# Performance work log

Measured on AMD Instinct MI355X. Metric: run time of the kernel, lower is better.

Reference implementation:

```python
import jax, jax.numpy as jnp
import numpy as np

N = 50000
E_RAND = 800000
F_IN = 128
HID = 128
HEADS = 8
LAYERS = 2
DH = HID // HEADS  # 16


def setup_inputs() -> dict:
    key = jax.random.key(0)
    ks = jax.random.split(key, 8)
    x = jax.random.normal(ks[0], (N, F_IN), dtype=jnp.float32)
    # random edges + self loops so every row of the segment-softmax is nonempty
    rnd = jax.random.randint(ks[1], (2, E_RAND), 0, N, dtype=jnp.int32)
    loops = jnp.tile(jnp.arange(N, dtype=jnp.int32), (2, 1))
    edge_idx = jnp.concatenate([rnd, loops], axis=1)  # [2, 850000]
    edge_vals = jnp.ones((edge_idx.shape[1],), dtype=jnp.float32)
    # glorot-style params
    enc_W = jax.random.normal(ks[2], (F_IN, HID), dtype=jnp.float32) * np.sqrt(2.0 / (F_IN + HID))
    enc_b = jnp.zeros((HID,), dtype=jnp.float32)
    W_stack = jax.random.normal(ks[3], (LAYERS, HEADS, HID, DH), dtype=jnp.float32) * np.sqrt(2.0 / (HID + DH))
    a_stack = jax.random.normal(ks[4], (LAYERS, HEADS, 2 * DH), dtype=jnp.float32) * np.sqrt(2.0 / (1 + 2 * DH))
    return {"x": x, "edge_idx": edge_idx, "edge_vals": edge_vals,
            "enc_W": enc_W, "enc_b": enc_b, "W_stack": W_stack, "a_stack": a_stack}


def _gat_layer(xin, row, col, edge_vals, W, a):
    # xin: [N, HID]; W: [H, HID, DH]; a: [H, 2*DH]
    n = xin.shape[0]
    h = jnp.einsum('nd,hdf->hnf', xin, W)            # [H, N, DH]
    a_src, a_dst = a[:, :DH], a[:, DH:]
    alpha_src = jnp.einsum('hnf,hf->hn', h, a_src)   # a . h[row] part
    alpha_dst = jnp.einsum('hnf,hf->hn', h, a_dst)   # a . h[col] part
    logits = edge_vals[None, :] * (alpha_src[:, row] + alpha_dst[:, col])  # [H, E]
    e = jnp.exp(jax.nn.leaky_relu(logits, 0.2))      # unnormalized attention
    rowsum = jax.ops.segment_sum(e.T, row, num_segments=n)               # [N, H]
    msg = e[:, :, None] * h[:, col, :]               # [H, E, DH]
    agg = jax.vmap(lambda m: jax.ops.segment_sum(m, row, num_segments=n))(msg)  # [H, N, DH]
    out = agg / rowsum.T[:, :, None]
    return jnp.transpose(out, (1, 0, 2)).reshape(n, -1)  # concat heads -> [N, HID]


def reference(x, edge_idx, edge_vals, enc_W, enc_b, W_stack, a_stack):
    row, col = edge_idx[0], edge_idx[1]
    xc = x @ enc_W + enc_b  # encoder
    L = W_stack.shape[0]
    for ell in range(L):
        out = _gat_layer(xc, row, col, edge_vals, W_stack[ell], a_stack[ell])
        if ell != L - 1:
            out = jax.nn.elu(out)  # feat_drop is identity in eval mode
        xc = out + xc if ell > 0 else out  # use_residual=True
    # single snapshot: stack over T=1 then permute(1,0,2) -> [N, 1, HID]
    return xc[:, None, :]
```

## Files before the change

kernel.cpp:

```cpp
#include <hip/hip_runtime.h>
#include <hip/hip_bf16.h>


typedef __attribute__((ext_vector_type(8))) short short8;
typedef __attribute__((ext_vector_type(4))) float floatx4;
typedef __attribute__((ext_vector_type(2))) float floatx2;

__device__ __forceinline__ unsigned f2u(float f) { return __float_as_uint(f); }
__device__ __forceinline__ float u2f(unsigned u) { return __uint_as_float(u); }
__device__ __forceinline__ unsigned short f2bf_rne(float x) {
    unsigned u = f2u(x);
    unsigned r = (u + 0x7FFF + ((u >> 16) & 1)) >> 16;
    return (unsigned short)r;
}
__device__ __forceinline__ float bf2f(unsigned short b) { return u2f(((unsigned)b) << 16); }


__global__ void hist_kernel(const int* __restrict__ row, int* __restrict__ deg,
                            int* __restrict__ rank, int E) {
    int e = blockIdx.x * 256 + threadIdx.x;
    if (e < E) rank[e] = atomicAdd(&deg[row[e]], 1);
}

__global__ void blocksum_kernel(const int* __restrict__ deg, int* __restrict__ bsum, int n) {
    __shared__ int sd[512];
    int t = threadIdx.x;
    int idx = blockIdx.x * 512 + t;
    sd[t] = (idx < n) ? deg[idx] : 0;
    __syncthreads();
    for (int off = 256; off; off >>= 1) {
        if (t < off) sd[t] += sd[t + off];
        __syncthreads();
    }
    if (t == 0) bsum[blockIdx.x] = sd[0];
}

__global__ void scanbsum_kernel(const int* __restrict__ bsum, int* __restrict__ boff,
                                int nb, int* __restrict__ rowptr, int n) {
    __shared__ int sd[128];
    int t = threadIdx.x;
    int v = (t < nb) ? bsum[t] : 0;
    sd[t] = v;
    __syncthreads();
    for (int off = 1; off < 128; off <<= 1) {
        int add = (t >= off) ? sd[t - off] : 0;
        __syncthreads();
        sd[t] += add;
        __syncthreads();
    }
    if (t < nb) boff[t] = sd[t] - v;
    if (t == nb - 1) rowptr[n] = sd[t];
}

__global__ void scanfinal_kernel(const int* __restrict__ deg, const int* __restrict__ boff,
                                 int* __restrict__ rowptr, int n) {
    __shared__ int sd[512];
    int t = threadIdx.x;
    int idx = blockIdx.x * 512 + t;
    int v = (idx < n) ? deg[idx] : 0;
    sd[t] = v;
    __syncthreads();
    for (int off = 1; off < 512; off <<= 1) {
        int add = (t >= off) ? sd[t - off] : 0;
        __syncthreads();
        sd[t] += add;
        __syncthreads();
    }
    if (idx < n) rowptr[idx] = sd[t] - v + boff[blockIdx.x];
}

__global__ void scatterperm_kernel(const int* __restrict__ row, const int* __restrict__ rank,
                                   const int* __restrict__ rowptr, int* __restrict__ perm,
                                   int E) {
    int e = blockIdx.x * 256 + threadIdx.x;
    if (e < E) perm[rowptr[row[e]] + rank[e]] = e;
}

__global__ void gathercv_kernel(const int* __restrict__ perm, const int* __restrict__ colv,
                                const float* __restrict__ ev, int2* __restrict__ csr_cv,
                                int E) {
    int s = blockIdx.x * 256 + threadIdx.x;
    if (s < E) {
        int e = perm[s];
        csr_cv[s] = make_int2(colv[e], __float_as_int(ev[e]));
    }
}


__global__ void pack_kernel(const float* __restrict__ encW, const float* __restrict__ Wstack,
                            short8* __restrict__ Wh, short8* __restrict__ Wl) {
    int idx = blockIdx.x * 256 + threadIdx.x;
    if (idx >= 3 * 2048) return;
    int mat = idx >> 11;
    int r = idx & 2047;
    int lane = r & 63;
    int tile = r >> 6;
    int ct = tile >> 2, kt = tile & 3;
    int ncol = ct * 16 + (lane & 15);
    int k0 = kt * 32 + ((lane >> 4) * 8);
    short8 hv, lv;
#pragma unroll
    for (int j = 0; j < 8; ++j) {
        int k = k0 + j;
        float w = (mat == 0)
            ? encW[k * 128 + ncol]
            : Wstack[(mat - 1) * 16384 + (ncol >> 4) * 2048 + k * 16 + (ncol & 15)];
        unsigned u = f2u(w);
        hv[j] = (short)(u >> 16);
        float hf = u2f(u & 0xFFFF0000u);
        float l = w - hf;
        lv[j] = (short)(f2u(l) >> 16);
    }
    Wh[idx] = hv;
    Wl[idx] = lv;
}


__global__ __launch_bounds__(256) void
gemm_mfma(const float* __restrict__ A, const short8* __restrict__ Bh,
          const short8* __restrict__ Bl, const float* __restrict__ bias,
          const float* __restrict__ avec, float* __restrict__ Cf,
          unsigned short* __restrict__ Cbf,
          float* __restrict__ asrc, float* __restrict__ adst, int n, int flags) {
    int wave = threadIdx.x >> 6;
    int lane = threadIdx.x & 63;
    int q = lane >> 4;
    int col = lane & 15;
    int n0w = blockIdx.x * 64 + wave * 16;

    int arow = min(n0w + col, n - 1);
    const float* Arow = A + (size_t)arow * 128;
    int kb = q * 8;
    short8 Ah[4], Al[4];
#pragma unroll
    for (int kt = 0; kt < 4; ++kt) {
        float4 f0 = *(const float4*)(Arow + kt * 32 + kb);
        float4 f1 = *(const float4*)(Arow + kt * 32 + kb + 4);
        float fv[8] = {f0.x, f0.y, f0.z, f0.w, f1.x, f1.y, f1.z, f1.w};
#pragma unroll
        for (int j = 0; j < 8; ++j) {
            unsigned u = f2u(fv[j]);
            Ah[kt][j] = (short)(u >> 16);
            float hf = u2f(u & 0xFFFF0000u);
            float l = fv[j] - hf;
            Al[kt][j] = (short)(f2u(l) >> 16);
        }
    }

    int nbase = n0w + q * 4;
#pragma unroll
    for (int ct = 0; ct < 8; ++ct) {
        short8 bh[4], bl[4];
#pragma unroll
        for (int kt = 0; kt < 4; ++kt) {
            bh[kt] = Bh[(ct * 4 + kt) * 64 + lane];
            bl[kt] = Bl[(ct * 4 + kt) * 64 + lane];
        }
        float bv = (flags & 1) ? bias[ct * 16 + col] : 0.f;
        floatx4 acc = {bv, bv, bv, bv};
#pragma unroll
        for (int kt = 0; kt < 4; ++kt) {
            acc = __builtin_amdgcn_mfma_f32_16x16x32_bf16(Ah[kt], bh[kt], acc, 0, 0, 0);
            acc = __builtin_amdgcn_mfma_f32_16x16x32_bf16(Al[kt], bh[kt], acc, 0, 0, 0);
            acc = __builtin_amdgcn_mfma_f32_16x16x32_bf16(Ah[kt], bl[kt], acc, 0, 0, 0);
        }
#pragma unroll
        for (int reg = 0; reg < 4; ++reg) {
            int node = nbase + reg;
            if (node < n) {
                if (flags & 4) Cbf[(size_t)node * 128 + ct * 16 + col] = f2bf_rne(acc[reg]);
                else           Cf[(size_t)node * 128 + ct * 16 + col] = acc[reg];
            }
        }
        if (flags & 2) {
            float a_s = avec[ct * 32 + col];
            float a_d = avec[ct * 32 + 16 + col];
#pragma unroll
            for (int reg = 0; reg < 4; ++reg) {
                float ps = acc[reg] * a_s;
                float pd = acc[reg] * a_d;
#pragma unroll
                for (int off = 8; off; off >>= 1) {
                    ps += __shfl_down(ps, off, 16);
                    pd += __shfl_down(pd, off, 16);
                }
                int node = nbase + reg;
                if (col == 0 && node < n) {
                    asrc[node * 8 + ct] = ps;
                    adst[node * 8 + ct] = pd;
                }
            }
        }
    }
}


__global__ __launch_bounds__(256) void
aggregate_kernel(const int* __restrict__ rowptr, const int2* __restrict__ cv,
                 const unsigned short* __restrict__ hbf,
                 const float* __restrict__ asrc, const float* __restrict__ adst,
                 const float* __restrict__ resid, float* __restrict__ out,
                 int mode, int n) {
    int wid = (blockIdx.x * 256 + threadIdx.x) >> 6;
    if (wid >= n) return;
    int lane = threadIdx.x & 63;
    int grp = lane >> 4;
    int l4 = lane & 15;
    int h = l4 >> 1;

    int s = rowptr[wid];
    int e = rowptr[wid + 1];
    float as_w = asrc[wid * 8 + h];

    floatx2 acc0 = {0.f, 0.f}, acc1 = {0.f, 0.f};
    floatx2 acc2 = {0.f, 0.f}, acc3 = {0.f, 0.f};
    float ws = 0.f;

#pragma unroll 4
    for (int j = s + grp; j < e; j += 4) {
        int2 cvj = cv[j];
        int c = cvj.x;
        float v = __int_as_float(cvj.y);
        float lg = v * (as_w + adst[c * 8 + h]);
        float lr = fmaxf(lg, 0.2f * lg);
        float w = __expf(lr);
        uint4 hv = *(const uint4*)(hbf + (size_t)c * 128 + l4 * 8);
        floatx2 w2 = {w, w};
        floatx2 p0 = {u2f(hv.x << 16), u2f(hv.x & 0xFFFF0000u)};
        floatx2 p1 = {u2f(hv.y << 16), u2f(hv.y & 0xFFFF0000u)};
        floatx2 p2 = {u2f(hv.z << 16), u2f(hv.z & 0xFFFF0000u)};
        floatx2 p3 = {u2f(hv.w << 16), u2f(hv.w & 0xFFFF0000u)};
        acc0 += w2 * p0;
        acc1 += w2 * p1;
        acc2 += w2 * p2;
        acc3 += w2 * p3;
        ws += w;
    }

    float a0 = acc0.x, a1 = acc0.y, a2 = acc1.x, a3 = acc1.y;
    float a4 = acc2.x, a5 = acc2.y, a6 = acc3.x, a7 = acc3.y;

#define RED4(x) x += __shfl_xor(x, 16); x += __shfl_xor(x, 32);
    RED4(a0) RED4(a1) RED4(a2) RED4(a3)
    RED4(a4) RED4(a5) RED4(a6) RED4(a7)
    RED4(ws)
#undef RED4

    if (grp == 0) {
        float inv = 1.0f / ws;
        float o[8] = {a0 * inv, a1 * inv, a2 * inv, a3 * inv,
                      a4 * inv, a5 * inv, a6 * inv, a7 * inv};
        size_t base = (size_t)wid * 128 + l4 * 8;
        if (mode == 0) {
#pragma unroll
            for (int k = 0; k < 8; ++k) o[k] = o[k] > 0.f ? o[k] : expm1f(o[k]);
        } else {
            float4 r0 = *(const float4*)(resid + base);
            float4 r1 = *(const float4*)(resid + base + 4);
            o[0] += r0.x; o[1] += r0.y; o[2] += r0.z; o[3] += r0.w;
            o[4] += r1.x; o[5] += r1.y; o[6] += r1.z; o[7] += r1.w;
        }
        float4 w0 = {o[0], o[1], o[2], o[3]};
        float4 w1 = {o[4], o[5], o[6], o[7]};
        *(float4*)(out + base) = w0;
        *(float4*)(out + base + 4) = w1;
    }
}


extern "C" void kernel_launch(void* const* d_in, const int* in_sizes, int n_in,
                              void* d_out, int out_size, void* d_ws, size_t ws_size,
                              hipStream_t stream) {
    const int N = in_sizes[0] / 128;
    const int E = in_sizes[2];

    const float* x      = (const float*)d_in[0];
    const int*   eidx   = (const int*)d_in[1];
    const float* ev     = (const float*)d_in[2];
    const float* encW   = (const float*)d_in[3];
    const float* encb   = (const float*)d_in[4];
    const float* Wstack = (const float*)d_in[5];
    const float* astack = (const float*)d_in[6];
    float* out = (float*)d_out;

    const int* row = eidx;
    const int* colv = eidx + E;

    char* p = (char*)d_ws;
    float* xc   = (float*)p; p += (size_t)N * 128 * 4;
    float* xcB  = (float*)p; p += (size_t)N * 128 * 4;
    unsigned short* hbf = (unsigned short*)p; p += (size_t)N * 128 * 2;
    float* asrc = (float*)p; p += (size_t)N * 8 * 4;
    float* adst = (float*)p; p += (size_t)N * 8 * 4;
    short8* Wh  = (short8*)p; p += 3 * 2048 * 16;
    short8* Wl  = (short8*)p; p += 3 * 2048 * 16;
    int2* csr_cv = (int2*)p; p += (size_t)E * 8;
    int* rowptr = (int*)p;   p += (size_t)(N + 1) * 4;
    int* deg    = (int*)p;   p += (size_t)N * 4;
    int* bsum   = (int*)p;   p += 128 * 4;
    int* boff   = (int*)p;

    int* rank = (int*)xc;
    int* perm = rank + E;

    const int NB = (N + 511) / 512;
    const int GB = (N + 63) / 64;
    const int AGG = (N + 3) / 4;
    const int EB = (E + 255) / 256;

    hipMemsetAsync(deg, 0, (size_t)N * 4, stream);
    hist_kernel<<<EB, 256, 0, stream>>>(row, deg, rank, E);
    blocksum_kernel<<<NB, 512, 0, stream>>>(deg, bsum, N);
    scanbsum_kernel<<<1, 128, 0, stream>>>(bsum, boff, NB, rowptr, N);
    scanfinal_kernel<<<NB, 512, 0, stream>>>(deg, boff, rowptr, N);
    scatterperm_kernel<<<EB, 256, 0, stream>>>(row, rank, rowptr, perm, E);
    gathercv_kernel<<<EB, 256, 0, stream>>>(perm, colv, ev, csr_cv, E);

    pack_kernel<<<24, 256, 0, stream>>>(encW, Wstack, Wh, Wl);

    gemm_mfma<<<GB, 256, 0, stream>>>(x, Wh, Wl, encb, nullptr, xc, nullptr,
                                      nullptr, nullptr, N, 1);

    gemm_mfma<<<GB, 256, 0, stream>>>(xc, Wh + 2048, Wl + 2048, nullptr, astack,
                                      nullptr, hbf, asrc, adst, N, 2 | 4);
    aggregate_kernel<<<AGG, 256, 0, stream>>>(rowptr, csr_cv, hbf, asrc, adst,
                                              nullptr, xcB, 0, N);

    gemm_mfma<<<GB, 256, 0, stream>>>(xcB, Wh + 4096, Wl + 4096, nullptr, astack + 256,
                                      nullptr, hbf, asrc, adst, N, 2 | 4);
    aggregate_kernel<<<AGG, 256, 0, stream>>>(rowptr, csr_cv, hbf, asrc, adst,
                                              xcB, out, 1, N);
}
```

Before: 312.2 us.

## Fuse weight packing into histogram, use atomic-offset scan, prefetch edges in aggregate

Merges the weight-packing kernel into the degree histogram launch as extra blocks. Replaces the three-kernel scan with a single kernel in which each block claims its base offset from a global cursor with an atomic. The resulting row ordering is not sorted by node but is still a valid CSR-like layout, since rows are addressed through rowstart plus degree. The aggregate loop now software-pipelines the edge (col, val) loads four at a time with a prefetch of the next batch, to hide gather latency. The goal is fewer launches and better memory-level parallelism, at the cost of irregular segment placement and more registers.

```diff
diff --git a/kernel.cpp b/kernel.cpp
--- a/kernel.cpp
+++ b/kernel.cpp
@@ -16,45 +16,47 @@
 __device__ __forceinline__ float bf2f(unsigned short b) { return u2f(((unsigned)b) << 16); }
 
 
-__global__ void hist_kernel(const int* __restrict__ row, int* __restrict__ deg,
-                            int* __restrict__ rank, int E) {
-    int e = blockIdx.x * 256 + threadIdx.x;
-    if (e < E) rank[e] = atomicAdd(&deg[row[e]], 1);
-}
-
-__global__ void blocksum_kernel(const int* __restrict__ deg, int* __restrict__ bsum, int n) {
+__global__ void histpack_kernel(const int* __restrict__ row, int* __restrict__ deg,
+                                int* __restrict__ rank, int E, int EB,
+                                const float* __restrict__ encW,
+                                const float* __restrict__ Wstack,
+                                short8* __restrict__ Wh, short8* __restrict__ Wl) {
+    int b = blockIdx.x;
+    if (b < EB) {
+        int e = b * 256 + threadIdx.x;
+        if (e < E) rank[e] = atomicAdd(&deg[row[e]], 1);
+        return;
+    }
+    int idx = (b - EB) * 256 + threadIdx.x;
+    if (idx >= 3 * 2048) return;
+    int mat = idx >> 11;
+    int r = idx & 2047;
+    int lane = r & 63;
+    int tile = r >> 6;
+    int ct = tile >> 2, kt = tile & 3;
+    int ncol = ct * 16 + (lane & 15);
+    int k0 = kt * 32 + ((lane >> 4) * 8);
+    short8 hv, lv;
+#pragma unroll
+    for (int j = 0; j < 8; ++j) {
+        int k = k0 + j;
+        float w = (mat == 0)
+            ? encW[k * 128 + ncol]
+            : Wstack[(mat - 1) * 16384 + (ncol >> 4) * 2048 + k * 16 + (ncol & 15)];
+        unsigned u = f2u(w);
+        hv[j] = (short)(u >> 16);
+        float hf = u2f(u & 0xFFFF0000u);
+        float l = w - hf;
+        lv[j] = (short)(f2u(l) >> 16);
+    }
+    Wh[idx] = hv;
+    Wl[idx] = lv;
+}
+
+__global__ void scan_atomic_kernel(const int* __restrict__ deg, int* __restrict__ rowstart,
+                                   int* __restrict__ gcursor, int n) {
     __shared__ int sd[512];
-    int t = threadIdx.x;
-    int idx = blockIdx.x * 512 + t;
-    sd[t] = (idx < n) ? deg[idx] : 0;
-    __syncthreads();
-    for (int off = 256; off; off >>= 1) {
-        if (t < off) sd[t] += sd[t + off];
-        __syncthreads();
-    }
-    if (t == 0) bsum[blockIdx.x] = sd[0];
-}
-
-__global__ void scanbsum_kernel(const int* __restrict__ bsum, int* __restrict__ boff,
-                                int nb, int* __restrict__ rowptr, int n) {
-    __shared__ int sd[128];
-    int t = threadIdx.x;
-    int v = (t < nb) ? bsum[t] : 0;
-    sd[t] = v;
-    __syncthreads();
-    for (int off = 1; off < 128; off <<= 1) {
-        int add = (t >= off) ? sd[t - off] : 0;
-        __syncthreads();
-        sd[t] += add;
-        __syncthreads();
-    }
-    if (t < nb) boff[t] = sd[t] - v;
-    if (t == nb - 1) rowptr[n] = sd[t];
-}
-
-__global__ void scanfinal_kernel(const int* __restrict__ deg, const int* __restrict__ boff,
-                                 int* __restrict__ rowptr, int n) {
-    __shared__ int sd[512];
+    __shared__ int sbase;
     int t = threadIdx.x;
     int idx = blockIdx.x * 512 + t;
     int v = (idx < n) ? deg[idx] : 0;
@@ -66,14 +68,16 @@
         sd[t] += add;
         __syncthreads();
     }
-    if (idx < n) rowptr[idx] = sd[t] - v + boff[blockIdx.x];
+    if (t == 511) sbase = atomicAdd(gcursor, sd[511]);
+    __syncthreads();
+    if (idx < n) rowstart[idx] = sbase + sd[t] - v;
 }
 
 __global__ void scatterperm_kernel(const int* __restrict__ row, const int* __restrict__ rank,
-                                   const int* __restrict__ rowptr, int* __restrict__ perm,
+                                   const int* __restrict__ rowstart, int* __restrict__ perm,
                                    int E) {
     int e = blockIdx.x * 256 + threadIdx.x;
-    if (e < E) perm[rowptr[row[e]] + rank[e]] = e;
+    if (e < E) perm[rowstart[row[e]] + rank[e]] = e;
 }
 
 __global__ void gathercv_kernel(const int* __restrict__ perm, const int* __restrict__ colv,
@@ -84,35 +88,6 @@
         int e = perm[s];
         csr_cv[s] = make_int2(colv[e], __float_as_int(ev[e]));
     }
-}
-
-
-__global__ void pack_kernel(const float* __restrict__ encW, const float* __restrict__ Wstack,
-                            short8* __restrict__ Wh, short8* __restrict__ Wl) {
-    int idx = blockIdx.x * 256 + threadIdx.x;
-    if (idx >= 3 * 2048) return;
-    int mat = idx >> 11;
-    int r = idx & 2047;
-    int lane = r & 63;
-    int tile = r >> 6;
-    int ct = tile >> 2, kt = tile & 3;
-    int ncol = ct * 16 + (lane & 15);
-    int k0 = kt * 32 + ((lane >> 4) * 8);
-    short8 hv, lv;
-#pragma unroll
-    for (int j = 0; j < 8; ++j) {
-        int k = k0 + j;
-        float w = (mat == 0)
-            ? encW[k * 128 + ncol]
-            : Wstack[(mat - 1) * 16384 + (ncol >> 4) * 2048 + k * 16 + (ncol & 15)];
-        unsigned u = f2u(w);
-        hv[j] = (short)(u >> 16);
-        float hf = u2f(u & 0xFFFF0000u);
-        float l = w - hf;
-        lv[j] = (short)(f2u(l) >> 16);
-    }
-    Wh[idx] = hv;
-    Wl[idx] = lv;
 }
 
 
@@ -195,8 +170,24 @@
 }
 
 
+#define PROC(W, JJ) if ((JJ) < e) {                                        \
+    int c = (W).x;                                                          \
+    float v = __int_as_float((W).y);                                        \
+    float lg = v * (as_w + adst[c * 8 + h]);                                \
+    float lr = fmaxf(lg, 0.2f * lg);                                        \
+    float w = __expf(lr);                                                   \
+    uint4 hv = *(const uint4*)(hbf + (size_t)c * 128 + l4 * 8);             \
+    floatx2 wv = {w, w};                                                    \
+    floatx2 p0 = {u2f(hv.x << 16), u2f(hv.x & 0xFFFF0000u)};                \
+    floatx2 p1 = {u2f(hv.y << 16), u2f(hv.y & 0xFFFF0000u)};                \
+    floatx2 p2 = {u2f(hv.z << 16), u2f(hv.z & 0xFFFF0000u)};                \
+    floatx2 p3 = {u2f(hv.w << 16), u2f(hv.w & 0xFFFF0000u)};                \
+    acc0 += wv * p0; acc1 += wv * p1; acc2 += wv * p2; acc3 += wv * p3;     \
+    ws += w; }
+
 __global__ __launch_bounds__(256) void
-aggregate_kernel(const int* __restrict__ rowptr, const int2* __restrict__ cv,
+aggregate_kernel(const int* __restrict__ rowstart, const int* __restrict__ degv,
+                 const int2* __restrict__ cv,
                  const unsigned short* __restrict__ hbf,
                  const float* __restrict__ asrc, const float* __restrict__ adst,
                  const float* __restrict__ resid, float* __restrict__ out,
@@ -208,33 +199,33 @@
     int l4 = lane & 15;
     int h = l4 >> 1;
 
-    int s = rowptr[wid];
-    int e = rowptr[wid + 1];
+    int s = rowstart[wid];
+    int e = s + degv[wid];
     float as_w = asrc[wid * 8 + h];
 
     floatx2 acc0 = {0.f, 0.f}, acc1 = {0.f, 0.f};
     floatx2 acc2 = {0.f, 0.f}, acc3 = {0.f, 0.f};
     float ws = 0.f;
 
-#pragma unroll 4
-    for (int j = s + grp; j < e; j += 4) {
-        int2 cvj = cv[j];
-        int c = cvj.x;
-        float v = __int_as_float(cvj.y);
-        float lg = v * (as_w + adst[c * 8 + h]);
-        float lr = fmaxf(lg, 0.2f * lg);
-        float w = __expf(lr);
-        uint4 hv = *(const uint4*)(hbf + (size_t)c * 128 + l4 * 8);
-        floatx2 w2 = {w, w};
-        floatx2 p0 = {u2f(hv.x << 16), u2f(hv.x & 0xFFFF0000u)};
-        floatx2 p1 = {u2f(hv.y << 16), u2f(hv.y & 0xFFFF0000u)};
-        floatx2 p2 = {u2f(hv.z << 16), u2f(hv.z & 0xFFFF0000u)};
-        floatx2 p3 = {u2f(hv.w << 16), u2f(hv.w & 0xFFFF0000u)};
-        acc0 += w2 * p0;
-        acc1 += w2 * p1;
-        acc2 += w2 * p2;
-        acc3 += w2 * p3;
-        ws += w;
+    int jb = s + grp;
+    int2 s0 = {0, 0}, s1 = {0, 0}, s2 = {0, 0}, s3 = {0, 0};
+    if (jb      < e) s0 = cv[jb];
+    if (jb + 4  < e) s1 = cv[jb + 4];
+    if (jb + 8  < e) s2 = cv[jb + 8];
+    if (jb + 12 < e) s3 = cv[jb + 12];
+
+    while (jb < e) {
+        int2 e0 = s0, e1 = s1, e2 = s2, e3 = s3;
+        int jn = jb + 16;
+        if (jn      < e) s0 = cv[jn];
+        if (jn + 4  < e) s1 = cv[jn + 4];
+        if (jn + 8  < e) s2 = cv[jn + 8];
+        if (jn + 12 < e) s3 = cv[jn + 12];
+        PROC(e0, jb)
+        PROC(e1, jb + 4)
+        PROC(e2, jb + 8)
+        PROC(e3, jb + 12)
+        jb = jn;
     }
 
     float a0 = acc0.x, a1 = acc0.y, a2 = acc1.x, a3 = acc1.y;
@@ -266,6 +257,7 @@
         *(float4*)(out + base + 4) = w1;
     }
 }
+#undef PROC
 
 
 extern "C" void kernel_launch(void* const* d_in, const int* in_sizes, int n_in,
@@ -295,10 +287,9 @@
     short8* Wh  = (short8*)p; p += 3 * 2048 * 16;
     short8* Wl  = (short8*)p; p += 3 * 2048 * 16;
     int2* csr_cv = (int2*)p; p += (size_t)E * 8;
-    int* rowptr = (int*)p;   p += (size_t)(N + 1) * 4;
+    int* rowstart = (int*)p; p += (size_t)N * 4;
     int* deg    = (int*)p;   p += (size_t)N * 4;
-    int* bsum   = (int*)p;   p += 128 * 4;
-    int* boff   = (int*)p;
+    int* gcursor = (int*)p;  p += 4;
 
     int* rank = (int*)xc;
     int* perm = rank + E;
@@ -308,26 +299,23 @@
     const int AGG = (N + 3) / 4;
     const int EB = (E + 255) / 256;
 
-    hipMemsetAsync(deg, 0, (size_t)N * 4, stream);
-    hist_kernel<<<EB, 256, 0, stream>>>(row, deg, rank, E);
-    blocksum_kernel<<<NB, 512, 0, stream>>>(deg, bsum, N);
-    scanbsum_kernel<<<1, 128, 0, stream>>>(bsum, boff, NB, rowptr, N);
-    scanfinal_kernel<<<NB, 512, 0, stream>>>(deg, boff, rowptr, N);
-    scatterperm_kernel<<<EB, 256, 0, stream>>>(row, rank, rowptr, perm, E);
+    hipMemsetAsync(deg, 0, (size_t)(N + 1) * 4, stream);
+    histpack_kernel<<<EB + 24, 256, 0, stream>>>(row, deg, rank, E, EB,
+                                                 encW, Wstack, Wh, Wl);
+    scan_atomic_kernel<<<NB, 512, 0, stream>>>(deg, rowstart, gcursor, N);
+    scatterperm_kernel<<<EB, 256, 0, stream>>>(row, rank, rowstart, perm, E);
     gathercv_kernel<<<EB, 256, 0, stream>>>(perm, colv, ev, csr_cv, E);
-
-    pack_kernel<<<24, 256, 0, stream>>>(encW, Wstack, Wh, Wl);
 
     gemm_mfma<<<GB, 256, 0, stream>>>(x, Wh, Wl, encb, nullptr, xc, nullptr,
                                       nullptr, nullptr, N, 1);
 
     gemm_mfma<<<GB, 256, 0, stream>>>(xc, Wh + 2048, Wl + 2048, nullptr, astack,
                                       nullptr, hbf, asrc, adst, N, 2 | 4);
-    aggregate_kernel<<<AGG, 256, 0, stream>>>(rowptr, csr_cv, hbf, asrc, adst,
+    aggregate_kernel<<<AGG, 256, 0, stream>>>(rowstart, deg, csr_cv, hbf, asrc, adst,
                                               nullptr, xcB, 0, N);
 
     gemm_mfma<<<GB, 256, 0, stream>>>(xcB, Wh + 4096, Wl + 4096, nullptr, astack + 256,
                                       nullptr, hbf, asrc, adst, N, 2 | 4);
-    aggregate_kernel<<<AGG, 256, 0, stream>>>(rowptr, csr_cv, hbf, asrc, adst,
+    aggregate_kernel<<<AGG, 256, 0, stream>>>(rowstart, deg, csr_cv, hbf, asrc, adst,
                                               xcB, out, 1, N);
 }
```

New measurement: 317.4 us. About the same (+1.7%).
